# Optimization experiments

Measured on AMD Instinct MI355X. Metric: run time of the kernel, lower is better.

Reference implementation:

```python
import jax, jax.numpy as jnp
from jax import lax
import numpy as np

B, T, S, U, E, V = 64, 50, 50, 1024, 100, 30001


def setup_inputs() -> dict:
    key = jax.random.key(0)
    ks = jax.random.split(key, 12)
    sc = 0.02
    return {
        "tokens": jax.random.randint(ks[0], (B, T), 0, V, dtype=jnp.int32),
        "memory": jax.random.normal(ks[1], (B, S, U), jnp.float32),
        "h0": jax.random.normal(ks[2], (B, U), jnp.float32),
        "c0": jax.random.normal(ks[3], (B, U), jnp.float32),
        "emb": jax.random.normal(ks[4], (V, E), jnp.float32) * sc,
        "Wx": jax.random.normal(ks[5], (E + U, 4 * U), jnp.float32) * sc,
        "Uh": jax.random.normal(ks[6], (U, 4 * U), jnp.float32) * sc,
        "b": jnp.zeros((4 * U,), jnp.float32),
        "Wm": jax.random.normal(ks[7], (U, U), jnp.float32) * sc,
        "Wa": jax.random.normal(ks[8], (2 * U, U), jnp.float32) * sc,
        "Wo": jax.random.normal(ks[9], (U, V), jnp.float32) * sc,
        "bo": jnp.zeros((V,), jnp.float32),
    }


def reference(tokens, memory, h0, c0, emb, Wx, Uh, b, Wm, Wa, Wo, bo):
    # Luong memory layer: keys = memory @ Wm (Dense(units, use_bias=False))
    keys = jnp.einsum("bsu,uk->bsk", memory, Wm)  # [B,S,U]
    x_emb = emb[tokens]                            # [B,T,E] teacher-forced inputs

    def step(carry, x_t):
        h, c, attn = carry
        # AttentionWrapper cell input: concat(embedding, prev attention)
        z = jnp.concatenate([x_t, attn], axis=-1) @ Wx + h @ Uh + b  # [B,4U]
        i, f, g, o = jnp.split(z, 4, axis=-1)  # keras gate order i,f,c,o
        c_new = jax.nn.sigmoid(f) * c + jax.nn.sigmoid(i) * jnp.tanh(g)
        h_new = jax.nn.sigmoid(o) * jnp.tanh(c_new)
        # Luong score: query (h_new) dot processed memory keys
        score = jnp.einsum("bu,bsu->bs", h_new, keys)
        align = jax.nn.softmax(score, axis=-1)
        ctx = jnp.einsum("bs,bsu->bu", align, memory)
        # attention_layer: Dense(units, use_bias=False) on concat(cell_out, ctx)
        attn_new = jnp.concatenate([h_new, ctx], axis=-1) @ Wa
        logits = attn_new @ Wo + bo  # output_layer
        return (h_new, c_new, attn_new), logits

    init = (h0, c0, jnp.zeros_like(h0))
    _, logits = lax.scan(step, init, jnp.swapaxes(x_emb, 0, 1))  # [T,B,V]
    return jnp.transpose(logits, (1, 0, 2))  # [B,T,V]
```

## Files before the change

### kernel.cpp

```cpp
#include <hip/hip_runtime.h>
#include <math.h>

#define B_  64
#define T_  50
#define S_  50
#define U_  1024
#define E_  100
#define V_  30001
#define U4_ 4096
#define VP_ 30080
#define HCSTR_ 131136

typedef __bf16 bf16_t;
typedef bf16_t bf16x8 __attribute__((ext_vector_type(8)));
typedef float  f32x4  __attribute__((ext_vector_type(4)));
typedef unsigned long long u64_t;

__device__ __forceinline__ float2 scload8(const float* p) {
    u64_t v = __hip_atomic_load((const u64_t*)p, __ATOMIC_RELAXED,
                                __HIP_MEMORY_SCOPE_SYSTEM);
    union { u64_t u; float2 f; } c; c.u = v; return c.f;
}
__device__ __forceinline__ void scstore8(float* p, float x, float y) {
    union { u64_t u; float2 f; } c; c.f = make_float2(x, y);
    __hip_atomic_store((u64_t*)p, c.u, __ATOMIC_RELAXED,
                       __HIP_MEMORY_SCOPE_SYSTEM);
}
__device__ __forceinline__ unsigned scload_u(const unsigned* p) {
    return __hip_atomic_load(p, __ATOMIC_RELAXED, __HIP_MEMORY_SCOPE_SYSTEM);
}
__device__ __forceinline__ void scadd_u(unsigned* p) {
    __hip_atomic_fetch_add(p, 1u, __ATOMIC_RELAXED, __HIP_MEMORY_SCOPE_SYSTEM);
}
__device__ __forceinline__ void vm_drain() {
    asm volatile("s_waitcnt vmcnt(0)" ::: "memory");
}
__device__ __forceinline__ void cbar() { asm volatile("" ::: "memory"); }

__global__ __launch_bounds__(256) void gemm128(
    const float* __restrict__ A, int lda,
    const float* __restrict__ Bm, int ldb,
    float* __restrict__ C, int ldc,
    int N, int K, const float* __restrict__ bias)
{
    __shared__ float As[8][132];
    __shared__ float Bs[8][132];

    const int n0  = blockIdx.x * 128;
    const int m0  = blockIdx.y * 128;
    const int tid = threadIdx.x;
    const int tx  = tid & 15, ty = tid >> 4;

    float acc[8][8];
#pragma unroll
    for (int i = 0; i < 8; ++i)
#pragma unroll
        for (int j = 0; j < 8; ++j) acc[i][j] = 0.f;

    const int ra = tid >> 1, ca = (tid & 1) * 4;
    const int rb = tid >> 5, cb = (tid & 31) * 4;
    const bool fast_b = ((ldb & 3) == 0) && (n0 + 128 <= N);

    for (int k0 = 0; k0 < K; k0 += 8) {
        const float* ap = &A[(size_t)(m0 + ra) * lda + k0 + ca];
        float4 av;
        if (k0 + 8 <= K) {
            av = *(const float4*)ap;
        } else {
            av.x = (k0 + ca + 0 < K) ? ap[0] : 0.f;
            av.y = (k0 + ca + 1 < K) ? ap[1] : 0.f;
            av.z = (k0 + ca + 2 < K) ? ap[2] : 0.f;
            av.w = (k0 + ca + 3 < K) ? ap[3] : 0.f;
        }
        As[ca + 0][ra] = av.x;
        As[ca + 1][ra] = av.y;
        As[ca + 2][ra] = av.z;
        As[ca + 3][ra] = av.w;

        float4 bv = make_float4(0.f, 0.f, 0.f, 0.f);
        if (k0 + rb < K) {
            const float* bp = &Bm[(size_t)(k0 + rb) * ldb];
            if (fast_b) {
                bv = *(const float4*)&bp[n0 + cb];
            } else {
                bv.x = (n0 + cb + 0 < N) ? bp[n0 + cb + 0] : 0.f;
                bv.y = (n0 + cb + 1 < N) ? bp[n0 + cb + 1] : 0.f;
                bv.z = (n0 + cb + 2 < N) ? bp[n0 + cb + 2] : 0.f;
                bv.w = (n0 + cb + 3 < N) ? bp[n0 + cb + 3] : 0.f;
            }
        }
        *(float4*)&Bs[rb][cb] = bv;
        __syncthreads();

#pragma unroll
        for (int kk = 0; kk < 8; ++kk) {
            float4 a0 = *(const float4*)&As[kk][ty * 4];
            float4 a1 = *(const float4*)&As[kk][64 + ty * 4];
            float4 b0 = *(const float4*)&Bs[kk][tx * 4];
            float4 b1 = *(const float4*)&Bs[kk][64 + tx * 4];
            float a_[8] = {a0.x, a0.y, a0.z, a0.w, a1.x, a1.y, a1.z, a1.w};
            float b_[8] = {b0.x, b0.y, b0.z, b0.w, b1.x, b1.y, b1.z, b1.w};
#pragma unroll
            for (int i = 0; i < 8; ++i)
#pragma unroll
                for (int j = 0; j < 8; ++j)
                    acc[i][j] = fmaf(a_[i], b_[j], acc[i][j]);
        }
        __syncthreads();
    }

#pragma unroll
    for (int i = 0; i < 8; ++i) {
        int row = m0 + ((i < 4) ? (ty * 4 + i) : (64 + ty * 4 + (i - 4)));
#pragma unroll
        for (int j = 0; j < 8; ++j) {
            int col = n0 + ((j < 4) ? (tx * 4 + j) : (64 + tx * 4 + (j - 4)));
            if (col < N) {
                float v = acc[i][j];
                if (bias) v += bias[col];
                C[(size_t)row * ldc + col] = v;
            }
        }
    }
}

__global__ void add_inplace(float* __restrict__ dst, const float* __restrict__ src, int n)
{
    int i = blockIdx.x * blockDim.x + threadIdx.x;
    if (i < n) dst[i] += src[i];
}

__global__ void gather_emb(const int* __restrict__ tokens,
                           const float* __restrict__ emb,
                           float* __restrict__ xe)
{
    const int r = blockIdx.x;
    const int e = threadIdx.x;
    if (e < E_) xe[(size_t)r * E_ + e] = emb[(size_t)tokens[r] * E_ + e];
}

__global__ __launch_bounds__(256) void transpose_wo(
    const float* __restrict__ wo, bf16_t* __restrict__ dst)
{
    __shared__ bf16_t tile[64][72];
    const int c0 = blockIdx.x * 64;
    const int k0 = blockIdx.y * 64;
    const int tx = threadIdx.x & 63, ty = threadIdx.x >> 6;

#pragma unroll
    for (int kk = ty; kk < 64; kk += 4) {
        const int col = c0 + tx;
        float v = (col < V_) ? wo[(size_t)(k0 + kk) * V_ + col] : 0.f;
        tile[kk][tx] = (bf16_t)v;
    }
    __syncthreads();
#pragma unroll
    for (int cc = ty; cc < 64; cc += 4)
        dst[(size_t)(c0 + cc) * 1024 + k0 + tx] = tile[tx][cc];
}

template <int OUT>
__global__ __launch_bounds__(256) void gemm_mfma_split(
    const float* __restrict__ A, int lda,
    const float* __restrict__ Bm, int ldb,
    float* __restrict__ C, int ldc, int K)
{
    __shared__ bf16_t As_h[128][40];
    __shared__ bf16_t As_l[128][40];
    __shared__ bf16_t Bs_h[128][40];
    __shared__ bf16_t Bs_l[128][40];

    const int n0  = blockIdx.x * 128;
    const int m0  = blockIdx.y * 128;
    const int tid = threadIdx.x;
    const int wave = tid >> 6, lane = tid & 63;
    const int wr = wave >> 1, wc = wave & 1;
    const int lr = lane & 15;
    const int lk = lane >> 4;

    f32x4 acc[4][4] = {};

    const int ar  = tid >> 1, ak = (tid & 1) * 16;
    const int bk0 = (tid >> 5) * 4, bc = (tid & 31) * 4;

    for (int k0 = 0; k0 < K; k0 += 32) {
        {
            const float* ap = &A[(size_t)(m0 + ar) * lda + k0 + ak];
            bf16x8 h0v, l0v, h1v, l1v;
#pragma unroll
            for (int q = 0; q < 2; ++q) {
                float4 v0 = *(const float4*)&ap[q * 8];
                float4 v1 = *(const float4*)&ap[q * 8 + 4];
                float xs[8] = {v0.x, v0.y, v0.z, v0.w, v1.x, v1.y, v1.z, v1.w};
#pragma unroll
                for (int e = 0; e < 8; ++e) {
                    bf16_t h = (bf16_t)xs[e];
                    if (q == 0) { h0v[e] = h; l0v[e] = (bf16_t)(xs[e] - (float)h); }
                    else        { h1v[e] = h; l1v[e] = (bf16_t)(xs[e] - (float)h); }
                }
            }
            *(bf16x8*)&As_h[ar][ak]     = h0v;
            *(bf16x8*)&As_h[ar][ak + 8] = h1v;
            *(bf16x8*)&As_l[ar][ak]     = l0v;
            *(bf16x8*)&As_l[ar][ak + 8] = l1v;
        }
        {
#pragma unroll
            for (int kk = 0; kk < 4; ++kk) {
                float4 v = *(const float4*)&Bm[(size_t)(k0 + bk0 + kk) * ldb + n0 + bc];
                float xs[4] = {v.x, v.y, v.z, v.w};
#pragma unroll
                for (int i = 0; i < 4; ++i) {
                    bf16_t h = (bf16_t)xs[i];
                    Bs_h[bc + i][bk0 + kk] = h;
                    Bs_l[bc + i][bk0 + kk] = (bf16_t)(xs[i] - (float)h);
                }
            }
        }
        __syncthreads();

        bf16x8 ah[4], alv[4], bh[4], bl[4];
#pragma unroll
        for (int m = 0; m < 4; ++m) {
            ah[m]  = *(const bf16x8*)&As_h[wr * 64 + m * 16 + lr][lk * 8];
            alv[m] = *(const bf16x8*)&As_l[wr * 64 + m * 16 + lr][lk * 8];
        }
#pragma unroll
        for (int n = 0; n < 4; ++n) {
            bh[n] = *(const bf16x8*)&Bs_h[wc * 64 + n * 16 + lr][lk * 8];
            bl[n] = *(const bf16x8*)&Bs_l[wc * 64 + n * 16 + lr][lk * 8];
        }
#pragma unroll
        for (int m = 0; m < 4; ++m)
#pragma unroll
            for (int n = 0; n < 4; ++n) {
                acc[m][n] = __builtin_amdgcn_mfma_f32_16x16x32_bf16(ah[m],  bh[n], acc[m][n], 0, 0, 0);
                acc[m][n] = __builtin_amdgcn_mfma_f32_16x16x32_bf16(ah[m],  bl[n], acc[m][n], 0, 0, 0);
                acc[m][n] = __builtin_amdgcn_mfma_f32_16x16x32_bf16(alv[m], bh[n], acc[m][n], 0, 0, 0);
            }
        __syncthreads();
    }

#pragma unroll
    for (int m = 0; m < 4; ++m) {
        const int row = m0 + wr * 64 + m * 16 + lk * 4;
#pragma unroll
        for (int n = 0; n < 4; ++n) {
            const int col = n0 + wc * 64 + n * 16 + lr;
#pragma unroll
            for (int r = 0; r < 4; ++r) {
                if (OUT == 0)
                    C[(size_t)(row + r) * ldc + col] = acc[m][n][r];
                else
                    ((bf16_t*)C)[(size_t)(row + r) * ldc + col] = (bf16_t)acc[m][n][r];
            }
        }
    }
}

__global__ __launch_bounds__(256) void zgemm_partial(
    const float* __restrict__ A, int lda,
    const float* __restrict__ Bm,
    float* __restrict__ zp)
{
    __shared__ float As[64][17];
    __shared__ float Bs[16][68];

    const int n0     = blockIdx.x * 64;
    const int ks     = blockIdx.y;
    const int k_base = ks * 256;
    const int tid    = threadIdx.x;
    const int tx     = tid & 15, ty = tid >> 4;

    float acc[4][4];
#pragma unroll
    for (int i = 0; i < 4; ++i)
#pragma unroll
        for (int j = 0; j < 4; ++j) acc[i][j] = 0.f;

    const int ra = tid >> 2, ca = (tid & 3) * 4;
    const int rb = tid >> 4, cb = (tid & 15) * 4;

    for (int kt = 0; kt < 16; ++kt) {
        const int k0 = k_base + kt * 16;
        float4 av = *(const float4*)&A[(size_t)ra * lda + k0 + ca];
        As[ra][ca + 0] = av.x;
        As[ra][ca + 1] = av.y;
        As[ra][ca + 2] = av.z;
        As[ra][ca + 3] = av.w;
        float4 bv = *(const float4*)&Bm[(size_t)(k0 + rb) * U4_ + n0 + cb];
        *(float4*)&Bs[rb][cb] = bv;
        __syncthreads();
#pragma unroll
        for (int kk = 0; kk < 16; ++kk) {
            float a_[4];
#pragma unroll
            for (int i = 0; i < 4; ++i) a_[i] = As[ty * 4 + i][kk];
            float4 bq = *(const float4*)&Bs[kk][tx * 4];
            float b_[4] = {bq.x, bq.y, bq.z, bq.w};
#pragma unroll
            for (int i = 0; i < 4; ++i)
#pragma unroll
                for (int j = 0; j < 4; ++j)
                    acc[i][j] = fmaf(a_[i], b_[j], acc[i][j]);
        }
        __syncthreads();
    }

#pragma unroll
    for (int i = 0; i < 4; ++i)
        *(float4*)&zp[((size_t)ks * 64 + ty * 4 + i) * U4_ + n0 + tx * 4] =
            make_float4(acc[i][0], acc[i][1], acc[i][2], acc[i][3]);
}

__global__ __launch_bounds__(512) void decoder_loop10(
    const float* __restrict__ zemb,
    const float* __restrict__ Wcomb,
    const float* __restrict__ keys,
    const float* __restrict__ memory,
    const float* __restrict__ c0,
    float* __restrict__ hcbuf,
    float* __restrict__ zp,
    float* __restrict__ hc_all,
    unsigned* flags)
{
    static __shared__ __attribute__((aligned(16))) char smem[154112];
    bf16_t* wfr = (bf16_t*)smem;
    float*  lA  = (float*)(smem + 131072);
    float*  tr  = (float*)(smem + 131072);
    float*  hs  = (float*)(smem + 149504);
    float*  sc  = (float*)(smem + 153600);
    float*  al  = (float*)(smem + 153856);

    const int beta = blockIdx.x;
    const int tid  = threadIdx.x;

    const int nt = beta & 63, ks = beta >> 6;
    const int koff = ks * 512;
    const int c0c  = nt * 64;

    for (int i = tid; i < 512 * 64; i += 512) {
        const int k = i >> 6, col = i & 63;
        const float w = Wcomb[(size_t)(koff + k) * U4_ + c0c + col];
        const bf16_t hi = (bf16_t)w;
        const bf16_t lo = (bf16_t)(w - (float)hi);
        const int ntile = col >> 4, lane_lo = col & 15;
        const int kk = k >> 5, kr = k & 31;
        const int lane = (kr >> 3) * 16 + lane_lo, j = kr & 7;
        const int base = ((ntile * 16 + kk) * 2) * 512 + lane * 8 + j;
        wfr[base]       = hi;
        wfr[base + 512] = lo;
    }

    const int b  = beta;
    const int u2 = tid * 2;
    float creg[2] = {0.f, 0.f};
    if (beta < 64) {
        float2 cv = *(const float2*)&c0[b * U_ + u2];
        creg[0] = cv.x;
        creg[1] = cv.y;
    }
    __syncthreads();

    const int w    = tid >> 6, l = tid & 63;
    const int mt   = w >> 1, ntb = (w & 1) * 2;
    const int arow = mt * 16 + (l & 15);
    const int aq   = l >> 4;
    const int aphys = arow * 36 + (((aq ^ (arow & 3)) & 3) << 3);
    const int sr = tid >> 3, sc4 = (tid & 7) * 4;
    const int sq = sc4 >> 3, srem = sc4 & 7;
    const int sphys = sr * 36 + (((sq ^ (sr & 3)) & 3) << 3) + srem;

    for (int t = 0; t < T_; ++t) {
        if (t) {
            {
                const unsigned tgt = 8u * (unsigned)t;
                const unsigned* fb = (ks < 2) ? &flags[512] : &flags[768];
                if (tid < 8) {
                    const unsigned* f = fb + tid * 32;
                    while (scload_u(f) < tgt) __builtin_amdgcn_s_sleep(1);
                }
                __syncthreads();
                cbar();
            }

            const float* apbase = &hcbuf[(size_t)(t - 1) * HCSTR_];
            {
                float4 av = *(const float4*)&apbase[(size_t)sr * 2048 + koff + sc4];
                *(float4*)&lA[sphys] = av;
            }
            __syncthreads();

            f32x4 acc[2] = {};
            for (int kk = 0; kk < 16; ++kk) {
                const int cur = kk & 1;
                float4 pre;
                if (kk < 15)
                    pre = *(const float4*)&apbase[(size_t)sr * 2048 + koff + (kk + 1) * 32 + sc4];

                const float* Ab = &lA[cur * 2304];
                float4 a0 = *(const float4*)&Ab[aphys];
                float4 a1 = *(const float4*)&Ab[aphys + 4];
                float xs[8] = {a0.x, a0.y, a0.z, a0.w, a1.x, a1.y, a1.z, a1.w};
                bf16x8 ah, alv;
#pragma unroll
                for (int e = 0; e < 8; ++e) {
                    bf16_t h = (bf16_t)xs[e];
                    ah[e]  = h;
                    alv[e] = (bf16_t)(xs[e] - (float)h);
                }
#pragma unroll
                for (int nn = 0; nn < 2; ++nn) {
                    const int fb2 = (((ntb + nn) * 16 + kk) * 2) * 512 + l * 8;
                    bf16x8 bh = *(const bf16x8*)&wfr[fb2];
                    bf16x8 bl = *(const bf16x8*)&wfr[fb2 + 512];
                    acc[nn] = __builtin_amdgcn_mfma_f32_16x16x32_bf16(ah, bh, acc[nn], 0, 0, 0);
                    acc[nn] = __builtin_amdgcn_mfma_f32_16x16x32_bf16(ah, bl, acc[nn], 0, 0, 0);
                    acc[nn] = __builtin_amdgcn_mfma_f32_16x16x32_bf16(alv, bh, acc[nn], 0, 0, 0);
                }
                if (kk < 15) {
                    *(float4*)&lA[(cur ^ 1) * 2304 + sphys] = pre;
                    __syncthreads();
                }
            }
            __syncthreads();

#pragma unroll
            for (int nn = 0; nn < 2; ++nn)
#pragma unroll
                for (int rr = 0; rr < 4; ++rr)
                    tr[(mt * 16 + (l >> 4) * 4 + rr) * 68 + (ntb + nn) * 16 + (l & 15)] =
                        acc[nn][rr];
            __syncthreads();

            {
                const int zb = tid >> 3, cg = (tid & 7) * 8;
                float4 r0 = *(const float4*)&tr[zb * 68 + cg];
                float4 r1 = *(const float4*)&tr[zb * 68 + cg + 4];
                float* zrow = &zp[((size_t)(ks * 64 + zb)) * U4_ + c0c + cg];
                scstore8(zrow + 0, r0.x, r0.y);
                scstore8(zrow + 2, r0.z, r0.w);
                scstore8(zrow + 4, r1.x, r1.y);
                scstore8(zrow + 6, r1.z, r1.w);
            }
            vm_drain();
            __syncthreads();
            if (tid == 0) scadd_u(&flags[(beta & 15) * 32]);
        }

        if (beta < 64) {
            if (t) {
                const unsigned tgt = 16u * (unsigned)t;
                if (tid < 16) {
                    const unsigned* f = &flags[tid * 32];
                    while (scload_u(f) < tgt) __builtin_amdgcn_s_sleep(1);
                }
                __syncthreads();
                cbar();
            }

            const float* ze = &zemb[((size_t)b * T_ + t) * U4_];
            float zgx[4], zgy[4];
#pragma unroll
            for (int g = 0; g < 4; ++g) {
                float2 a = *(const float2*)&ze[g * U_ + u2];
                zgx[g] = a.x;
                zgy[g] = a.y;
            }
#pragma unroll
            for (int s = 0; s < 4; ++s) {
#pragma unroll
                for (int g = 0; g < 4; ++g) {
                    float2 v = scload8(&zp[((size_t)s * 64 + b) * U4_ + g * U_ + u2]);
                    zgx[g] += v.x;
                    zgy[g] += v.y;
                }
            }

            const float six = 1.f / (1.f + expf(-zgx[0]));
            const float sfx = 1.f / (1.f + expf(-zgx[1]));
            const float tgx = tanhf(zgx[2]);
            const float sox = 1.f / (1.f + expf(-zgx[3]));
            const float cnx = sfx * creg[0] + six * tgx;
            creg[0] = cnx;
            const float hnx = sox * tanhf(cnx);

            const float siy = 1.f / (1.f + expf(-zgy[0]));
            const float sfy = 1.f / (1.f + expf(-zgy[1]));
            const float tgy = tanhf(zgy[2]);
            const float soy = 1.f / (1.f + expf(-zgy[3]));
            const float cny = sfy * creg[1] + siy * tgy;
            creg[1] = cny;
            const float hny = soy * tanhf(cny);

            float* hcb_t = &hcbuf[(size_t)t * HCSTR_];
            hs[u2]     = hnx;
            hs[u2 + 1] = hny;
            scstore8(&hcb_t[b * 2048 + u2], hnx, hny);
            *(float2*)&hc_all[((size_t)b * T_ + t) * 2048 + u2] =
                make_float2(hnx, hny);
            vm_drain();
            __syncthreads();
            if (tid == 0) scadd_u(&flags[512 + (b & 7) * 32]);

            const int lane = tid & 63, wv = tid >> 6;
            for (int s = wv; s < S_; s += 8) {
                const float* kp = &keys[((size_t)b * S_ + s) * U_ + lane * 16];
                const float* hp = &hs[lane * 16];
                float p = 0.f;
#pragma unroll
                for (int q = 0; q < 4; ++q) {
                    float4 kv = *(const float4*)&kp[q * 4];
                    float4 hv = *(const float4*)&hp[q * 4];
                    p = fmaf(hv.x, kv.x, p);
                    p = fmaf(hv.y, kv.y, p);
                    p = fmaf(hv.z, kv.z, p);
                    p = fmaf(hv.w, kv.w, p);
                }
#pragma unroll
                for (int off = 32; off > 0; off >>= 1)
                    p += __shfl_xor(p, off);
                if (lane == 0) sc[s] = p;
            }
            __syncthreads();

            if (tid < 64) {
                float v = (tid < S_) ? sc[tid] : -INFINITY;
                float m = v;
#pragma unroll
                for (int off = 32; off > 0; off >>= 1)
                    m = fmaxf(m, __shfl_xor(m, off));
                float e = (tid < S_) ? expf(v - m) : 0.f;
                float ssum = e;
#pragma unroll
                for (int off = 32; off > 0; off >>= 1)
                    ssum += __shfl_xor(ssum, off);
                if (tid < S_) al[tid] = e / ssum;
            }
            __syncthreads();

            {
                const float2* mp = (const float2*)&memory[(size_t)b * S_ * U_];
                float cx = 0.f, cy = 0.f;
#pragma unroll 10
                for (int s = 0; s < S_; ++s) {
                    float2 mv = mp[s * 512 + tid];
                    const float a = al[s];
                    cx = fmaf(a, mv.x, cx);
                    cy = fmaf(a, mv.y, cy);
                }
                scstore8(&hcb_t[b * 2048 + U_ + u2], cx, cy);
                *(float2*)&hc_all[((size_t)b * T_ + t) * 2048 + U_ + u2] =
                    make_float2(cx, cy);
            }
            vm_drain();
            __syncthreads();
            if (tid == 0) scadd_u(&flags[768 + (b & 7) * 32]);
        }
    }
}

__global__ __launch_bounds__(256) void gemm_wo_mfma2(
    const bf16_t* __restrict__ A,
    const bf16_t* __restrict__ Bt,
    const float*  __restrict__ bias,
    float* __restrict__ C)
{
    __shared__ bf16_t As[128][40];
    __shared__ bf16_t Bs[128][40];

    const int n0  = blockIdx.x * 128;
    const int m0  = blockIdx.y * 128;
    const int tid = threadIdx.x;
    const int wave = tid >> 6, lane = tid & 63;
    const int wr = wave >> 1, wc = wave & 1;
    const int lr = lane & 15;
    const int lk = lane >> 4;

    f32x4 acc[4][4] = {};

    const int ar = tid >> 1, ak = (tid & 1) * 16;
    const int br = tid >> 1, bk = (tid & 1) * 16;

    for (int k0 = 0; k0 < U_; k0 += 32) {
        {
            const bf16_t* ap = &A[(size_t)(m0 + ar) * U_ + k0 + ak];
            *(bf16x8*)&As[ar][ak]     = *(const bf16x8*)ap;
            *(bf16x8*)&As[ar][ak + 8] = *(const bf16x8*)(ap + 8);
        }
        {
            const bf16_t* bp = &Bt[(size_t)(n0 + br) * 1024 + k0 + bk];
            *(bf16x8*)&Bs[br][bk]     = *(const bf16x8*)bp;
            *(bf16x8*)&Bs[br][bk + 8] = *(const bf16x8*)(bp + 8);
        }
        __syncthreads();

        bf16x8 af[4], bf[4];
#pragma unroll
        for (int m = 0; m < 4; ++m)
            af[m] = *(const bf16x8*)&As[wr * 64 + m * 16 + lr][lk * 8];
#pragma unroll
        for (int n = 0; n < 4; ++n)
            bf[n] = *(const bf16x8*)&Bs[wc * 64 + n * 16 + lr][lk * 8];
#pragma unroll
        for (int m = 0; m < 4; ++m)
#pragma unroll
            for (int n = 0; n < 4; ++n)
                acc[m][n] = __builtin_amdgcn_mfma_f32_16x16x32_bf16(
                    af[m], bf[n], acc[m][n], 0, 0, 0);
        __syncthreads();
    }

#pragma unroll
    for (int m = 0; m < 4; ++m) {
        const int row = m0 + wr * 64 + m * 16 + lk * 4;
#pragma unroll
        for (int n = 0; n < 4; ++n) {
            const int col = n0 + wc * 64 + n * 16 + lr;
            if (col < V_) {
                const float bb = bias[col];
#pragma unroll
                for (int r = 0; r < 4; ++r)
                    C[(size_t)(row + r) * V_ + col] = acc[m][n][r] + bb;
            }
        }
    }
}

extern "C" void kernel_launch(void* const* d_in, const int* in_sizes, int n_in,
                              void* d_out, int out_size, void* d_ws, size_t ws_size,
                              hipStream_t stream)
{
    const int*   tokens = (const int*)  d_in[0];
    const float* memory = (const float*)d_in[1];
    const float* h0     = (const float*)d_in[2];
    const float* c0     = (const float*)d_in[3];
    const float* emb    = (const float*)d_in[4];
    const float* Wx     = (const float*)d_in[5];
    const float* Uh     = (const float*)d_in[6];
    const float* bvec   = (const float*)d_in[7];
    const float* Wm     = (const float*)d_in[8];
    const float* Wa     = (const float*)d_in[9];
    const float* Wo     = (const float*)d_in[10];
    const float* bo     = (const float*)d_in[11];
    float* out = (float*)d_out;

    float* ws = (float*)d_ws;
    size_t off = 0;
    float*   Wcomb  = ws + off; off += (size_t)2048 * U4_;
    float*   keys   = ws + off; off += (size_t)B_ * S_ * U_;
    float*   hc_all = ws + off; off += (size_t)B_ * T_ * 2048;
    float*   zp     = ws + off; off += (size_t)4 * B_ * U4_;
    float*   x_emb  = ws + off; off += (size_t)B_ * T_ * E_;
    unsigned* flags = (unsigned*)(ws + off); off += 1024;
    bf16_t*  wo_t   = (bf16_t*)(ws + off); off += (size_t)VP_ * 1024 / 2;

    float* zemb  = out;
    float* hcbuf = out + (size_t)3200 * U4_;
    bf16_t* abf  = (bf16_t*)Wcomb;

    (void)ws_size;
    (void)hipMemsetAsync(flags, 0, 1024 * sizeof(unsigned), stream);

    gather_emb<<<B_ * T_, 128, 0, stream>>>(tokens, emb, x_emb);
    gemm128<<<dim3(32, 25), 256, 0, stream>>>(
        x_emb, E_, Wx, U4_, zemb, U4_, U4_, E_, bvec);
    gemm_mfma_split<0><<<dim3(32, 16), 256, 0, stream>>>(
        Wa, U_, Wx + (size_t)E_ * U4_, U4_, Wcomb, U4_, U_);
    add_inplace<<<(1024 * U4_) / 256, 256, 0, stream>>>(Wcomb, Uh, 1024 * U4_);
    gemm_mfma_split<0><<<dim3(8, 25), 256, 0, stream>>>(
        memory, U_, Wm, U_, keys, U_, U_);
    zgemm_partial<<<dim3(64, 4), 256, 0, stream>>>(h0, U_, Uh, zp);
    transpose_wo<<<dim3(VP_ / 64, 1024 / 64), 256, 0, stream>>>(Wo, wo_t);

    decoder_loop10<<<256, 512, 0, stream>>>(
        zemb, Wcomb, keys, memory, c0, hcbuf, zp, hc_all, flags);

    gemm_mfma_split<1><<<dim3(8, 25), 256, 0, stream>>>(
        hc_all, 2048, Wa, U_, (float*)abf, U_, 2048);
    gemm_wo_mfma2<<<dim3(VP_ / 128, 25), 256, 0, stream>>>(abf, wo_t, bo, out);
}
```

Measured before the change: 2.213 ms.

## Use MFMA for embedding GEMM, drop LDS staging in decoder, double-buffer Wo GEMM

Replaces the scalar fp32 embedding GEMM with the MFMA split GEMM. It pads the embedding input to K=128 and folds the bias in as a ones column plus an extra weight row. The decoder's recurrent GEMM now reads hc state directly from global memory into registers with prefetching, which removes the LDS staging and the per-iteration barriers. The output vocab GEMM gains double-buffered shared memory so the next tile's global loads overlap the current MFMAs. The padded Wx is stored in spare output buffer space, which adds an extra pad kernel launch.

```diff
diff --git a/kernel.cpp b/kernel.cpp
--- a/kernel.cpp
+++ b/kernel.cpp
@@ -37,106 +37,36 @@
 }
 __device__ __forceinline__ void cbar() { asm volatile("" ::: "memory"); }
 
-__global__ __launch_bounds__(256) void gemm128(
-    const float* __restrict__ A, int lda,
-    const float* __restrict__ Bm, int ldb,
-    float* __restrict__ C, int ldc,
-    int N, int K, const float* __restrict__ bias)
-{
-    __shared__ float As[8][132];
-    __shared__ float Bs[8][132];
-
-    const int n0  = blockIdx.x * 128;
-    const int m0  = blockIdx.y * 128;
-    const int tid = threadIdx.x;
-    const int tx  = tid & 15, ty = tid >> 4;
-
-    float acc[8][8];
-#pragma unroll
-    for (int i = 0; i < 8; ++i)
-#pragma unroll
-        for (int j = 0; j < 8; ++j) acc[i][j] = 0.f;
-
-    const int ra = tid >> 1, ca = (tid & 1) * 4;
-    const int rb = tid >> 5, cb = (tid & 31) * 4;
-    const bool fast_b = ((ldb & 3) == 0) && (n0 + 128 <= N);
-
-    for (int k0 = 0; k0 < K; k0 += 8) {
-        const float* ap = &A[(size_t)(m0 + ra) * lda + k0 + ca];
-        float4 av;
-        if (k0 + 8 <= K) {
-            av = *(const float4*)ap;
-        } else {
-            av.x = (k0 + ca + 0 < K) ? ap[0] : 0.f;
-            av.y = (k0 + ca + 1 < K) ? ap[1] : 0.f;
-            av.z = (k0 + ca + 2 < K) ? ap[2] : 0.f;
-            av.w = (k0 + ca + 3 < K) ? ap[3] : 0.f;
-        }
-        As[ca + 0][ra] = av.x;
-        As[ca + 1][ra] = av.y;
-        As[ca + 2][ra] = av.z;
-        As[ca + 3][ra] = av.w;
-
-        float4 bv = make_float4(0.f, 0.f, 0.f, 0.f);
-        if (k0 + rb < K) {
-            const float* bp = &Bm[(size_t)(k0 + rb) * ldb];
-            if (fast_b) {
-                bv = *(const float4*)&bp[n0 + cb];
-            } else {
-                bv.x = (n0 + cb + 0 < N) ? bp[n0 + cb + 0] : 0.f;
-                bv.y = (n0 + cb + 1 < N) ? bp[n0 + cb + 1] : 0.f;
-                bv.z = (n0 + cb + 2 < N) ? bp[n0 + cb + 2] : 0.f;
-                bv.w = (n0 + cb + 3 < N) ? bp[n0 + cb + 3] : 0.f;
-            }
-        }
-        *(float4*)&Bs[rb][cb] = bv;
-        __syncthreads();
-
-#pragma unroll
-        for (int kk = 0; kk < 8; ++kk) {
-            float4 a0 = *(const float4*)&As[kk][ty * 4];
-            float4 a1 = *(const float4*)&As[kk][64 + ty * 4];
-            float4 b0 = *(const float4*)&Bs[kk][tx * 4];
-            float4 b1 = *(const float4*)&Bs[kk][64 + tx * 4];
-            float a_[8] = {a0.x, a0.y, a0.z, a0.w, a1.x, a1.y, a1.z, a1.w};
-            float b_[8] = {b0.x, b0.y, b0.z, b0.w, b1.x, b1.y, b1.z, b1.w};
-#pragma unroll
-            for (int i = 0; i < 8; ++i)
-#pragma unroll
-                for (int j = 0; j < 8; ++j)
-                    acc[i][j] = fmaf(a_[i], b_[j], acc[i][j]);
-        }
-        __syncthreads();
-    }
-
-#pragma unroll
-    for (int i = 0; i < 8; ++i) {
-        int row = m0 + ((i < 4) ? (ty * 4 + i) : (64 + ty * 4 + (i - 4)));
-#pragma unroll
-        for (int j = 0; j < 8; ++j) {
-            int col = n0 + ((j < 4) ? (tx * 4 + j) : (64 + tx * 4 + (j - 4)));
-            if (col < N) {
-                float v = acc[i][j];
-                if (bias) v += bias[col];
-                C[(size_t)row * ldc + col] = v;
-            }
-        }
-    }
-}
-
 __global__ void add_inplace(float* __restrict__ dst, const float* __restrict__ src, int n)
 {
     int i = blockIdx.x * blockDim.x + threadIdx.x;
     if (i < n) dst[i] += src[i];
 }
 
-__global__ void gather_emb(const int* __restrict__ tokens,
-                           const float* __restrict__ emb,
-                           float* __restrict__ xe)
+__global__ void gather_emb_pad(const int* __restrict__ tokens,
+                               const float* __restrict__ emb,
+                               float* __restrict__ xe)
 {
     const int r = blockIdx.x;
     const int e = threadIdx.x;
-    if (e < E_) xe[(size_t)r * E_ + e] = emb[(size_t)tokens[r] * E_ + e];
+    float v;
+    if (e < E_)       v = emb[(size_t)tokens[r] * E_ + e];
+    else if (e == E_) v = 1.f;
+    else              v = 0.f;
+    xe[(size_t)r * 128 + e] = v;
+}
+
+__global__ void pad_wx(const float* __restrict__ Wx,
+                       const float* __restrict__ bvec,
+                       float* __restrict__ dst)
+{
+    const int col = blockIdx.x * 256 + threadIdx.x;
+    const int row = blockIdx.y;
+    float v;
+    if (row < E_)       v = Wx[(size_t)row * U4_ + col];
+    else if (row == E_) v = bvec[col];
+    else                v = 0.f;
+    dst[(size_t)row * U4_ + col] = v;
 }
 
 __global__ __launch_bounds__(256) void transpose_wo(
@@ -313,7 +243,7 @@
             make_float4(acc[i][0], acc[i][1], acc[i][2], acc[i][3]);
 }
 
-__global__ __launch_bounds__(512) void decoder_loop10(
+__global__ __launch_bounds__(512) void decoder_loop11(
     const float* __restrict__ zemb,
     const float* __restrict__ Wcomb,
     const float* __restrict__ keys,
@@ -324,13 +254,12 @@
     float* __restrict__ hc_all,
     unsigned* flags)
 {
-    static __shared__ __attribute__((aligned(16))) char smem[154112];
+    static __shared__ __attribute__((aligned(16))) char smem[153088];
     bf16_t* wfr = (bf16_t*)smem;
-    float*  lA  = (float*)(smem + 131072);
     float*  tr  = (float*)(smem + 131072);
-    float*  hs  = (float*)(smem + 149504);
-    float*  sc  = (float*)(smem + 153600);
-    float*  al  = (float*)(smem + 153856);
+    float*  hs  = (float*)(smem + 148480);
+    float*  sc  = (float*)(smem + 152576);
+    float*  al  = (float*)(smem + 152832);
 
     const int beta = blockIdx.x;
     const int tid  = threadIdx.x;
@@ -362,14 +291,11 @@
     }
     __syncthreads();
 
-    const int w    = tid >> 6, l = tid & 63;
-    const int mt   = w >> 1, ntb = (w & 1) * 2;
+    const int w  = tid >> 6, l = tid & 63;
+    const int mt = w >> 1, ntb = (w & 1) * 2;
     const int arow = mt * 16 + (l & 15);
     const int aq   = l >> 4;
-    const int aphys = arow * 36 + (((aq ^ (arow & 3)) & 3) << 3);
-    const int sr = tid >> 3, sc4 = (tid & 7) * 4;
-    const int sq = sc4 >> 3, srem = sc4 & 7;
-    const int sphys = sr * 36 + (((sq ^ (sr & 3)) & 3) << 3) + srem;
+    const size_t abase = (size_t)arow * 2048 + koff + aq * 8;
 
     for (int t = 0; t < T_; ++t) {
         if (t) {
@@ -384,24 +310,20 @@
                 cbar();
             }
 
-            const float* apbase = &hcbuf[(size_t)(t - 1) * HCSTR_];
-            {
-                float4 av = *(const float4*)&apbase[(size_t)sr * 2048 + koff + sc4];
-                *(float4*)&lA[sphys] = av;
-            }
-            __syncthreads();
+            const float* ap = &hcbuf[(size_t)(t - 1) * HCSTR_ + abase];
 
             f32x4 acc[2] = {};
+            float4 ca0 = *(const float4*)&ap[0];
+            float4 ca1 = *(const float4*)&ap[4];
+#pragma unroll
             for (int kk = 0; kk < 16; ++kk) {
-                const int cur = kk & 1;
-                float4 pre;
-                if (kk < 15)
-                    pre = *(const float4*)&apbase[(size_t)sr * 2048 + koff + (kk + 1) * 32 + sc4];
-
-                const float* Ab = &lA[cur * 2304];
-                float4 a0 = *(const float4*)&Ab[aphys];
-                float4 a1 = *(const float4*)&Ab[aphys + 4];
-                float xs[8] = {a0.x, a0.y, a0.z, a0.w, a1.x, a1.y, a1.z, a1.w};
+                float4 pa0, pa1;
+                if (kk < 15) {
+                    pa0 = *(const float4*)&ap[(kk + 1) * 32];
+                    pa1 = *(const float4*)&ap[(kk + 1) * 32 + 4];
+                }
+                float xs[8] = {ca0.x, ca0.y, ca0.z, ca0.w,
+                               ca1.x, ca1.y, ca1.z, ca1.w};
                 bf16x8 ah, alv;
 #pragma unroll
                 for (int e = 0; e < 8; ++e) {
@@ -418,12 +340,9 @@
                     acc[nn] = __builtin_amdgcn_mfma_f32_16x16x32_bf16(ah, bl, acc[nn], 0, 0, 0);
                     acc[nn] = __builtin_amdgcn_mfma_f32_16x16x32_bf16(alv, bh, acc[nn], 0, 0, 0);
                 }
-                if (kk < 15) {
-                    *(float4*)&lA[(cur ^ 1) * 2304 + sphys] = pre;
-                    __syncthreads();
-                }
-            }
-            __syncthreads();
+                ca0 = pa0;
+                ca1 = pa1;
+            }
 
 #pragma unroll
             for (int nn = 0; nn < 2; ++nn)
@@ -560,14 +479,14 @@
     }
 }
 
-__global__ __launch_bounds__(256) void gemm_wo_mfma2(
+__global__ __launch_bounds__(256) void gemm_wo_mfma3(
     const bf16_t* __restrict__ A,
     const bf16_t* __restrict__ Bt,
     const float*  __restrict__ bias,
     float* __restrict__ C)
 {
-    __shared__ bf16_t As[128][40];
-    __shared__ bf16_t Bs[128][40];
+    __shared__ bf16_t As[2][128][40];
+    __shared__ bf16_t Bs[2][128][40];
 
     const int n0  = blockIdx.x * 128;
     const int m0  = blockIdx.y * 128;
@@ -580,34 +499,48 @@
     f32x4 acc[4][4] = {};
 
     const int ar = tid >> 1, ak = (tid & 1) * 16;
-    const int br = tid >> 1, bk = (tid & 1) * 16;
+    const bf16_t* apb = &A[(size_t)(m0 + ar) * U_ + ak];
+    const bf16_t* bpb = &Bt[(size_t)(n0 + ar) * U_ + ak];
+
+    {
+        *(bf16x8*)&As[0][ar][ak]     = *(const bf16x8*)&apb[0];
+        *(bf16x8*)&As[0][ar][ak + 8] = *(const bf16x8*)&apb[8];
+        *(bf16x8*)&Bs[0][ar][ak]     = *(const bf16x8*)&bpb[0];
+        *(bf16x8*)&Bs[0][ar][ak + 8] = *(const bf16x8*)&bpb[8];
+    }
+    __syncthreads();
 
     for (int k0 = 0; k0 < U_; k0 += 32) {
-        {
-            const bf16_t* ap = &A[(size_t)(m0 + ar) * U_ + k0 + ak];
-            *(bf16x8*)&As[ar][ak]     = *(const bf16x8*)ap;
-            *(bf16x8*)&As[ar][ak + 8] = *(const bf16x8*)(ap + 8);
-        }
-        {
-            const bf16_t* bp = &Bt[(size_t)(n0 + br) * 1024 + k0 + bk];
-            *(bf16x8*)&Bs[br][bk]     = *(const bf16x8*)bp;
-            *(bf16x8*)&Bs[br][bk + 8] = *(const bf16x8*)(bp + 8);
-        }
-        __syncthreads();
+        const int cur = (k0 >> 5) & 1;
+        bf16x8 na0, na1, nb0, nb1;
+        const bool more = (k0 + 32 < U_);
+        if (more) {
+            na0 = *(const bf16x8*)&apb[k0 + 32];
+            na1 = *(const bf16x8*)&apb[k0 + 40];
+            nb0 = *(const bf16x8*)&bpb[k0 + 32];
+            nb1 = *(const bf16x8*)&bpb[k0 + 40];
+        }
 
         bf16x8 af[4], bf[4];
 #pragma unroll
         for (int m = 0; m < 4; ++m)
-            af[m] = *(const bf16x8*)&As[wr * 64 + m * 16 + lr][lk * 8];
+            af[m] = *(const bf16x8*)&As[cur][wr * 64 + m * 16 + lr][lk * 8];
 #pragma unroll
         for (int n = 0; n < 4; ++n)
-            bf[n] = *(const bf16x8*)&Bs[wc * 64 + n * 16 + lr][lk * 8];
+            bf[n] = *(const bf16x8*)&Bs[cur][wc * 64 + n * 16 + lr][lk * 8];
 #pragma unroll
         for (int m = 0; m < 4; ++m)
 #pragma unroll
             for (int n = 0; n < 4; ++n)
                 acc[m][n] = __builtin_amdgcn_mfma_f32_16x16x32_bf16(
                     af[m], bf[n], acc[m][n], 0, 0, 0);
+
+        if (more) {
+            *(bf16x8*)&As[cur ^ 1][ar][ak]     = na0;
+            *(bf16x8*)&As[cur ^ 1][ar][ak + 8] = na1;
+            *(bf16x8*)&Bs[cur ^ 1][ar][ak]     = nb0;
+            *(bf16x8*)&Bs[cur ^ 1][ar][ak + 8] = nb1;
+        }
         __syncthreads();
     }
 
@@ -651,20 +584,22 @@
     float*   keys   = ws + off; off += (size_t)B_ * S_ * U_;
     float*   hc_all = ws + off; off += (size_t)B_ * T_ * 2048;
     float*   zp     = ws + off; off += (size_t)4 * B_ * U4_;
-    float*   x_emb  = ws + off; off += (size_t)B_ * T_ * E_;
+    float*   x_emb  = ws + off; off += (size_t)B_ * T_ * 128;
     unsigned* flags = (unsigned*)(ws + off); off += 1024;
     bf16_t*  wo_t   = (bf16_t*)(ws + off); off += (size_t)VP_ * 1024 / 2;
 
-    float* zemb  = out;
-    float* hcbuf = out + (size_t)3200 * U4_;
-    bf16_t* abf  = (bf16_t*)Wcomb;
+    float* zemb   = out;
+    float* hcbuf  = out + (size_t)3200 * U4_;
+    float* wx_pad = out + (size_t)3200 * U4_ + (size_t)T_ * HCSTR_;
+    bf16_t* abf   = (bf16_t*)Wcomb;
 
     (void)ws_size;
     (void)hipMemsetAsync(flags, 0, 1024 * sizeof(unsigned), stream);
 
-    gather_emb<<<B_ * T_, 128, 0, stream>>>(tokens, emb, x_emb);
-    gemm128<<<dim3(32, 25), 256, 0, stream>>>(
-        x_emb, E_, Wx, U4_, zemb, U4_, U4_, E_, bvec);
+    gather_emb_pad<<<B_ * T_, 128, 0, stream>>>(tokens, emb, x_emb);
+    pad_wx<<<dim3(U4_ / 256, 128), 256, 0, stream>>>(Wx, bvec, wx_pad);
+    gemm_mfma_split<0><<<dim3(32, 25), 256, 0, stream>>>(
+        x_emb, 128, wx_pad, U4_, zemb, U4_, 128);
     gemm_mfma_split<0><<<dim3(32, 16), 256, 0, stream>>>(
         Wa, U_, Wx + (size_t)E_ * U4_, U4_, Wcomb, U4_, U_);
     add_inplace<<<(1024 * U4_) / 256, 256, 0, stream>>>(Wcomb, Uh, 1024 * U4_);
@@ -673,10 +608,10 @@
     zgemm_partial<<<dim3(64, 4), 256, 0, stream>>>(h0, U_, Uh, zp);
     transpose_wo<<<dim3(VP_ / 64, 1024 / 64), 256, 0, stream>>>(Wo, wo_t);
 
-    decoder_loop10<<<256, 512, 0, stream>>>(
+    decoder_loop11<<<256, 512, 0, stream>>>(
         zemb, Wcomb, keys, memory, c0, hcbuf, zp, hc_all, flags);
 
     gemm_mfma_split<1><<<dim3(8, 25), 256, 0, stream>>>(
         hc_all, 2048, Wa, U_, (float*)abf, U_, 2048);
-    gemm_wo_mfma2<<<dim3(VP_ / 128, 25), 256, 0, stream>>>(abf, wo_t, bo, out);
-}
+    gemm_wo_mfma3<<<dim3(VP_ / 128, 25), 256, 0, stream>>>(abf, wo_t, bo, out);
+}
```

Result: faster. 2.137 ms, median of 2 (-3.4%).
